# Kernel optimization log

Measured on AMD Instinct MI355X. Metric: run time of the kernel, lower is better.

## Reference

```python
import jax, jax.numpy as jnp
import numpy as np

B, D, N, OUT, H = 32768, 256, 4, 512, 4
DH = D // H


def _layer_norm(x, g, b, eps=1e-5):
    mu = jnp.mean(x, axis=-1, keepdims=True)
    var = jnp.mean(jnp.square(x - mu), axis=-1, keepdims=True)
    return (x - mu) * jax.lax.rsqrt(var + eps) * g + b


def setup_inputs() -> dict:
    key = jax.random.key(0)
    ks = jax.random.split(key, 32)
    s = lambda i, shape, scale=0.02: (jax.random.normal(ks[i], shape, jnp.float32) * scale)
    inp = {
        'w0': jax.random.normal(ks[0], (B, D), jnp.float32),
        'w1': jax.random.normal(ks[1], (B, D), jnp.float32),
        'w2': jax.random.normal(ks[2], (B, D), jnp.float32),
        'w3': jax.random.normal(ks[3], (B, D), jnp.float32),
        'regime': jax.random.uniform(ks[4], (B, 4), jnp.float32),
        'tf_weights': jnp.array([0.5, 1.0, 1.5, 2.0], jnp.float32),
        'in_proj_w': s(5, (3 * D, D)),
        'in_proj_b': s(6, (3 * D,)),
        'out_proj_w': s(7, (D, D)),
        'out_proj_b': s(8, (D,)),
        'ln1_g': jnp.ones((D,), jnp.float32),
        'ln1_b': jnp.zeros((D,), jnp.float32),
        'sg_w': s(9, (D, 4)),
        'sg_b': s(10, (D,)),
        'sb_w': s(11, (D, 4)),
        'sb_b': s(12, (D,)),
        'f1_w': s(13, (2 * OUT, D * N)),
        'f1_b': s(14, (2 * OUT,)),
        'f2_w': s(15, (OUT, 2 * OUT)),
        'f2_b': s(16, (OUT,)),
        'ln2_g': jnp.ones((OUT,), jnp.float32),
        'ln2_b': jnp.zeros((OUT,), jnp.float32),
        'a1_w': s(17, (128, D * N)),
        'a1_b': s(18, (128,)),
        'a2_w': s(19, (1, 128)),
        'a2_b': s(20, (1,)),
    }
    return inp


def _forward(w0, w1, w2, w3, regime, tf_weights, in_proj_w, in_proj_b,
             out_proj_w, out_proj_b, ln1_g, ln1_b, sg_w, sg_b, sb_w, sb_b,
             f1_w, f1_b, f2_w, f2_b, ln2_g, ln2_b, a1_w, a1_b, a2_w, a2_b):
    weights = jax.nn.softmax(tf_weights)  # [N]
    wav = jnp.stack([w0, w1, w2, w3], axis=1)  # [B, N, D]
    weighted = wav * weights[None, :, None]    # [B, N, D]
    query = weighted[:, 0, :]                  # [B, D]

    # MultiheadAttention: q_len=1, kv_len=N, H heads
    wq, wk, wv = in_proj_w[:D], in_proj_w[D:2 * D], in_proj_w[2 * D:]
    bq, bk, bv = in_proj_b[:D], in_proj_b[D:2 * D], in_proj_b[2 * D:]
    q = (query @ wq.T + bq).reshape(B, H, DH)              # [B, H, Dh]
    k = (weighted @ wk.T + bk).reshape(B, N, H, DH)        # [B, N, H, Dh]
    v = (weighted @ wv.T + bv).reshape(B, N, H, DH)
    scores = jnp.einsum('bhd,bnhd->bhn', q, k) / jnp.sqrt(jnp.float32(DH))
    attn = jax.nn.softmax(scores, axis=-1)                 # [B, H, N]
    ctx = jnp.einsum('bhn,bnhd->bhd', attn, v).reshape(B, D)
    attn_out = ctx @ out_proj_w.T + out_proj_b             # [B, D]

    entry = _layer_norm(query + attn_out, ln1_g, ln1_b)    # [B, D]
    gamma = regime @ sg_w.T + sg_b
    beta = regime @ sb_w.T + sb_b
    entry = entry * (1.0 + gamma) + beta                   # FiLM

    cat = jnp.concatenate([entry, weighted[:, 1, :], weighted[:, 2, :], weighted[:, 3, :]], axis=-1)  # [B, D*N]
    h = jax.nn.gelu(cat @ f1_w.T + f1_b, approximate=False)
    fused = _layer_norm(h @ f2_w.T + f2_b, ln2_g, ln2_b)   # [B, OUT]

    a = jax.nn.gelu(cat @ a1_w.T + a1_b, approximate=False)
    alignment = jax.nn.sigmoid(a @ a2_w.T + a2_b)          # [B, 1]
    return fused, alignment


def reference(w0, w1, w2, w3, regime, tf_weights, in_proj_w, in_proj_b,
              out_proj_w, out_proj_b, ln1_g, ln1_b, sg_w, sg_b, sb_w, sb_b,
              f1_w, f1_b, f2_w, f2_b, ln2_g, ln2_b, a1_w, a1_b, a2_w, a2_b):
    return _forward(w0, w1, w2, w3, regime, tf_weights, in_proj_w, in_proj_b,
                    out_proj_w, out_proj_b, ln1_g, ln1_b, sg_w, sg_b, sb_w, sb_b,
                    f1_w, f1_b, f2_w, f2_b, ln2_g, ln2_b, a1_w, a1_b, a2_w, a2_b)
```

## Files before the change

### kernel.cpp

```cpp
#include <hip/hip_runtime.h>
#include <math.h>

#define NB 32768

typedef unsigned short u16;
typedef __attribute__((ext_vector_type(4))) float f32x4;
typedef __attribute__((ext_vector_type(8))) short bf16x8;

__device__ __forceinline__ float bf2f(u16 u){ return __uint_as_float(((unsigned int)u)<<16); }
__device__ __forceinline__ u16 f2bf(float f){
    unsigned int x = __float_as_uint(f);
    x += 0x7fffu + ((x>>16)&1u);
    return (u16)(x>>16);
}
__device__ __forceinline__ float gelu_f(float x){
    float z = fabsf(x) * 0.70710678118654752f;
    float t = __builtin_amdgcn_rcpf(1.0f + 0.3275911f*z);
    float p = t*(0.254829592f + t*(-0.284496736f + t*(1.421413741f + t*(-1.453152027f + t*1.061405429f))));
    float e = __expf(-z*z);
    float erf_abs = 1.0f - p*e;
    float erfv = copysignf(erf_abs, x);
    return 0.5f*x*(1.0f + erfv);
}

__device__ __forceinline__ void gload16(const void* g, void* l){
    __builtin_amdgcn_global_load_lds(
        (const __attribute__((address_space(1))) unsigned int*)g,
        (__attribute__((address_space(3))) unsigned int*)l, 16, 0, 0);
}

__global__ __launch_bounds__(256) void prepconv_kernel(
    const float* __restrict__ w0, const float* __restrict__ w1,
    const float* __restrict__ w2, const float* __restrict__ w3,
    const float* __restrict__ tfw, u16* __restrict__ wcat,
    const float* __restrict__ ipw_s, u16* __restrict__ ipw_d,
    const float* __restrict__ op_s,  u16* __restrict__ op_d,
    const float* __restrict__ f1_s,  u16* __restrict__ f1_d,
    const float* __restrict__ f2_s,  u16* __restrict__ f2_d,
    const float* __restrict__ a1_s,  u16* __restrict__ a1_d)
{
    const int blk = blockIdx.x, tid = threadIdx.x;
    if (blk < 8192){
        float t0=tfw[0], t1=tfw[1], t2=tfw[2], t3=tfw[3];
        float m = fmaxf(fmaxf(t0,t1), fmaxf(t2,t3));
        float e0=expf(t0-m), e1=expf(t1-m), e2=expf(t2-m), e3=expf(t3-m);
        float inv = 1.0f/(e0+e1+e2+e3);
        float s0=e0*inv, s1=e1*inv, s2=e2*inv, s3=e3*inv;

        int idx = blk*256 + tid;
        int b  = idx >> 6;
        int d4 = (idx & 63) << 2;
        size_t src = (size_t)b*256 + d4;
        float4 a0 = *reinterpret_cast<const float4*>(w0 + src);
        float4 a1 = *reinterpret_cast<const float4*>(w1 + src);
        float4 a2 = *reinterpret_cast<const float4*>(w2 + src);
        float4 a3 = *reinterpret_cast<const float4*>(w3 + src);
        size_t dst = (size_t)b*1024 + d4;
        ushort4 o;
        o.x=f2bf(a0.x*s0); o.y=f2bf(a0.y*s0); o.z=f2bf(a0.z*s0); o.w=f2bf(a0.w*s0);
        *reinterpret_cast<ushort4*>(wcat + dst) = o;
        o.x=f2bf(a1.x*s1); o.y=f2bf(a1.y*s1); o.z=f2bf(a1.z*s1); o.w=f2bf(a1.w*s1);
        *reinterpret_cast<ushort4*>(wcat + dst + 256) = o;
        o.x=f2bf(a2.x*s2); o.y=f2bf(a2.y*s2); o.z=f2bf(a2.z*s2); o.w=f2bf(a2.w*s2);
        *reinterpret_cast<ushort4*>(wcat + dst + 512) = o;
        o.x=f2bf(a3.x*s3); o.y=f2bf(a3.y*s3); o.z=f2bf(a3.z*s3); o.w=f2bf(a3.w*s3);
        *reinterpret_cast<ushort4*>(wcat + dst + 768) = o;
    } else {
        int i = (blk - 8192)*256 + tid;
        const float* s; u16* d; int off;
        if      (i < 49152)  { s=ipw_s; d=ipw_d; off=i; }
        else if (i < 65536)  { s=op_s;  d=op_d;  off=i-49152; }
        else if (i < 327680) { s=f1_s;  d=f1_d;  off=i-65536; }
        else if (i < 458752) { s=f2_s;  d=f2_d;  off=i-327680; }
        else                 { s=a1_s;  d=a1_d;  off=i-458752; }
        float4 v = reinterpret_cast<const float4*>(s)[off];
        ushort4 o; o.x=f2bf(v.x); o.y=f2bf(v.y); o.z=f2bf(v.z); o.w=f2bf(v.w);
        reinterpret_cast<ushort4*>(d)[off] = o;
    }
}

template<int ACT>
__global__ __launch_bounds__(256) void mgemm_kernel(
    const u16* __restrict__ A, int lda,
    const u16* __restrict__ W, int ldw,
    const float* __restrict__ bias,
    u16* __restrict__ C, int ldc, int K,
    const float* __restrict__ a2w, const float* __restrict__ a2b, float* __restrict__ aln)
{
    __shared__ __align__(16) u16 sA[4096];
    __shared__ __align__(16) u16 sB[4096];

    const int tid  = threadIdx.x;
    const int lane = tid & 63;
    const int wid  = tid >> 6;
    const int wr   = wid >> 1, wc = wid & 1;
    const int row0 = blockIdx.x << 7, col0 = blockIdx.y << 7;

    const int e0 = tid << 3,          r0s = e0 >> 5, c0s = e0 & 31;
    const int e1 = (256 + tid) << 3,  r1s = e1 >> 5, c1s = e1 & 31;
    const u16* gA0 = A + (size_t)(row0 + r0s)*lda + c0s;
    const u16* gA1 = A + (size_t)(row0 + r1s)*lda + c1s;
    const u16* gB0 = W + (size_t)(col0 + r0s)*ldw + c0s;
    const u16* gB1 = W + (size_t)(col0 + r1s)*ldw + c1s;
    u16* lA0 = sA + (wid << 9);
    u16* lA1 = sA + 2048 + (wid << 9);
    u16* lB0 = sB + (wid << 9);
    u16* lB1 = sB + 2048 + (wid << 9);

    const int la  = lane & 15;
    const int lk  = (lane >> 4) << 3;
    const int hi4 = (lane >> 4) << 2;
    const u16* rA = sA + (((wr << 6) + la) << 5) + lk;
    const u16* rB = sB + (((wc << 6) + la) << 5) + lk;

    f32x4 acc[4][4];
    {
        f32x4 binit[4];
        #pragma unroll
        for (int n=0;n<4;n++){
            float4 b4 = *reinterpret_cast<const float4*>(bias + col0 + (wc<<6) + (n<<4) + hi4);
            binit[n] = (f32x4){b4.x, b4.y, b4.z, b4.w};
        }
        #pragma unroll
        for (int m=0;m<4;m++)
            #pragma unroll
            for (int n=0;n<4;n++) acc[m][n] = binit[n];
    }

    for (int k0 = 0; k0 < K; k0 += 32){
        gload16(gA0 + k0, lA0);
        gload16(gA1 + k0, lA1);
        gload16(gB0 + k0, lB0);
        gload16(gB1 + k0, lB1);
        __syncthreads();
        bf16x8 af[4], bf[4];
        #pragma unroll
        for (int m=0;m<4;m++) af[m] = *reinterpret_cast<const bf16x8*>(rA + (m << 9));
        #pragma unroll
        for (int n=0;n<4;n++) bf[n] = *reinterpret_cast<const bf16x8*>(rB + (n << 9));
        #pragma unroll
        for (int m=0;m<4;m++)
            #pragma unroll
            for (int n=0;n<4;n++)
                acc[m][n] = __builtin_amdgcn_mfma_f32_16x16x32_bf16(bf[n], af[m], acc[m][n], 0, 0, 0);
        __syncthreads();
    }

    if (ACT == 2){
        float w4[4][4];
        #pragma unroll
        for (int n=0;n<4;n++){
            float4 t4 = *reinterpret_cast<const float4*>(a2w + (wc<<6) + (n<<4) + hi4);
            w4[n][0]=t4.x; w4[n][1]=t4.y; w4[n][2]=t4.z; w4[n][3]=t4.w;
        }
        float* red = reinterpret_cast<float*>(sA);
        #pragma unroll
        for (int m=0;m<4;m++){
            float p = 0.f;
            #pragma unroll
            for (int n=0;n<4;n++){
                f32x4 v = acc[m][n];
                p += gelu_f(v[0])*w4[n][0] + gelu_f(v[1])*w4[n][1]
                   + gelu_f(v[2])*w4[n][2] + gelu_f(v[3])*w4[n][3];
            }
            red[(((wr<<6) + (m<<4) + la) << 3) + (wc<<2) + (lane>>4)] = p;
        }
        __syncthreads();
        if (tid < 128){
            float s = 0.f;
            #pragma unroll
            for (int k2=0;k2<8;k2++) s += red[(tid<<3)+k2];
            aln[row0 + tid] = 1.0f/(1.0f + __expf(-(s + a2b[0])));
        }
        return;
    }

    #pragma unroll
    for (int m=0;m<4;m++){
        const int grow = row0 + (wr << 6) + (m << 4) + la;
        u16* crow = C + (size_t)grow*ldc + col0 + (wc << 6) + hi4;
        #pragma unroll
        for (int n=0;n<4;n++){
            f32x4 v = acc[m][n];
            float x0=v[0], x1=v[1], x2=v[2], x3=v[3];
            if (ACT == 1){ x0=gelu_f(x0); x1=gelu_f(x1); x2=gelu_f(x2); x3=gelu_f(x3); }
            ushort4 o; o.x=f2bf(x0); o.y=f2bf(x1); o.z=f2bf(x2); o.w=f2bf(x3);
            *reinterpret_cast<ushort4*>(crow + (n << 4)) = o;
        }
    }
}

template<int ACT>
__global__ __launch_bounds__(512) void gemm256p_kernel(
    const u16* __restrict__ A, int lda,
    const u16* __restrict__ W, int ldw,
    const float* __restrict__ bias,
    u16* __restrict__ C, int ldc, int K)
{
    __shared__ __align__(16) u16 sT[65536];

    const int tid  = threadIdx.x;
    const int lane = tid & 63;
    const int wid  = tid >> 6;
    const int wr   = wid >> 2;
    const int wc   = wid & 3;
    const int row0 = blockIdx.x << 8, col0 = blockIdx.y << 8;

    const int la = lane & 15;
    const int hi = lane >> 4;

    f32x4 acc[8][4];
    {
        f32x4 binit[4];
        #pragma unroll
        for (int n=0;n<4;n++){
            float4 b4 = *reinterpret_cast<const float4*>(bias + col0 + (wc<<6) + (n<<4) + (hi<<2));
            binit[n] = (f32x4){b4.x, b4.y, b4.z, b4.w};
        }
        #pragma unroll
        for (int m=0;m<8;m++)
            #pragma unroll
            for (int n=0;n<4;n++) acc[m][n] = binit[n];
    }

    const int rs = (wid << 4) + (lane >> 3);
    const int cs = ((lane & 7) ^ ((lane >> 3) & 7)) << 3;
    const u16* gA0 = A + (size_t)(row0 + rs)*lda + cs;
    const u16* gA1 = gA0 + (size_t)128*lda;
    const u16* gB0 = W + (size_t)(col0 + rs)*ldw + cs;
    const u16* gB1 = gB0 + (size_t)128*ldw;
    const int ldsw = (wid << 4) * 64;

    const int cph0 = (hi ^ (la & 7)) << 3;
    const u16* rAbase = sT + ((wr << 7) + la)*64;
    const u16* rBbase = sT + 16384 + ((wc << 6) + la)*64;

    const int NT = K >> 6;

    gload16(gB0, sT + 16384 + ldsw);          gload16(gB0 + 8*(size_t)ldw, sT + 16384 + ldsw + 512);
    gload16(gB1, sT + 24576 + ldsw);          gload16(gB1 + 8*(size_t)ldw, sT + 24576 + ldsw + 512);
    gload16(gA0, sT + ldsw);                  gload16(gA0 + 8*(size_t)lda, sT + ldsw + 512);
    gload16(gA1, sT + 8192 + ldsw);           gload16(gA1 + 8*(size_t)lda, sT + 8192 + ldsw + 512);

#define STG(GP, LD, DOFF) \
        gload16(GP + kb, sT + bn + (DOFF) + ldsw); \
        gload16(GP + kb + 8*(size_t)(LD), sT + bn + (DOFF) + ldsw + 512);

#define DSRA(MH, CO) { \
        const u16* rA_ = rAbase + b + ((MH) << 12) + (CO); \
        af[0] = *reinterpret_cast<const bf16x8*>(rA_); \
        af[1] = *reinterpret_cast<const bf16x8*>(rA_ + 1024); \
        af[2] = *reinterpret_cast<const bf16x8*>(rA_ + 2048); \
        af[3] = *reinterpret_cast<const bf16x8*>(rA_ + 3072); }

#define DSRB(CO) { \
        const u16* rB_ = rBbase + b + (CO); \
        bf[0] = *reinterpret_cast<const bf16x8*>(rB_); \
        bf[1] = *reinterpret_cast<const bf16x8*>(rB_ + 1024); \
        bf[2] = *reinterpret_cast<const bf16x8*>(rB_ + 2048); \
        bf[3] = *reinterpret_cast<const bf16x8*>(rB_ + 3072); }

#define MFMA16(MB) { \
        _Pragma("unroll") \
        for (int m=0;m<4;m++){ \
            _Pragma("unroll") \
            for (int n=0;n<4;n++) \
                acc[(MB)+m][n] = __builtin_amdgcn_mfma_f32_16x16x32_bf16(bf[n], af[m], acc[(MB)+m][n], 0,0,0); \
        } }

    for (int t = 0; t < NT; ++t){
        const int b  = (t & 1) << 15;
        const int bn = b ^ 32768;
        const bool stg = (t + 1 < NT);
        const int kb = (t + 1) << 6;
        bf16x8 af[4], bf[4];
        const int co0 = cph0;
        const int co1 = cph0 ^ 32;

        asm volatile("s_waitcnt vmcnt(0)" ::: "memory");
        __builtin_amdgcn_s_barrier();
        __builtin_amdgcn_sched_barrier(0);
        DSRB(co0)
        DSRA(0, co0)
        if (stg){ STG(gB0, ldw, 16384) }
        MFMA16(0)
        DSRA(1, co0)
        if (stg){ STG(gB1, ldw, 24576) }
        __builtin_amdgcn_sched_barrier(0);
        __builtin_amdgcn_s_barrier();
        __builtin_amdgcn_sched_barrier(0);
        MFMA16(4)
        DSRB(co1)
        DSRA(0, co1)
        if (stg){ STG(gA0, lda, 0) }
        __builtin_amdgcn_sched_barrier(0);
        __builtin_amdgcn_s_barrier();
        __builtin_amdgcn_sched_barrier(0);
        MFMA16(0)
        DSRA(1, co1)
        if (stg){ STG(gA1, lda, 8192) }
        __builtin_amdgcn_sched_barrier(0);
        __builtin_amdgcn_s_barrier();
        __builtin_amdgcn_sched_barrier(0);
        MFMA16(4)
    }
#undef STG
#undef DSRA
#undef DSRB
#undef MFMA16

    #pragma unroll
    for (int m=0;m<8;m++){
        const int grow = row0 + (wr << 7) + (m << 4) + la;
        u16* crow = C + (size_t)grow*ldc + col0 + (wc << 6) + (hi << 2);
        #pragma unroll
        for (int n=0;n<4;n++){
            f32x4 v = acc[m][n];
            float x0=v[0], x1=v[1], x2=v[2], x3=v[3];
            if (ACT == 1){ x0=gelu_f(x0); x1=gelu_f(x1); x2=gelu_f(x2); x3=gelu_f(x3); }
            ushort4 o; o.x=f2bf(x0); o.y=f2bf(x1); o.z=f2bf(x2); o.w=f2bf(x3);
            *reinterpret_cast<ushort4*>(crow + (n << 4)) = o;
        }
    }
}

__global__ __launch_bounds__(256) void attn_kernel(
    const u16* __restrict__ q, const u16* __restrict__ kv,
    u16* __restrict__ ctx)
{
    __shared__ float sQ[256], sK[1024], sV[1024], sS[16], sA[16];
    const int b = blockIdx.x, t = threadIdx.x;
    sQ[t] = bf2f(q[(size_t)b*256 + t]);
    #pragma unroll
    for (int n=0;n<4;n++){
        sK[n*256+t] = bf2f(kv[(size_t)b*2048 + n*512 + t]);
        sV[n*256+t] = bf2f(kv[(size_t)b*2048 + n*512 + 256 + t]);
    }
    __syncthreads();
    if (t < 16){
        int h = t>>2, n = t&3;
        float s = 0.f;
        const int o = h*64;
        #pragma unroll
        for (int dh=0; dh<64; ++dh) s += sQ[o+dh]*sK[n*256+o+dh];
        sS[t] = s * 0.125f;
    }
    __syncthreads();
    if (t < 4){
        float a0=sS[t*4+0], a1=sS[t*4+1], a2=sS[t*4+2], a3=sS[t*4+3];
        float m = fmaxf(fmaxf(a0,a1), fmaxf(a2,a3));
        float e0=expf(a0-m), e1=expf(a1-m), e2=expf(a2-m), e3=expf(a3-m);
        float inv = 1.0f/(e0+e1+e2+e3);
        sA[t*4+0]=e0*inv; sA[t*4+1]=e1*inv; sA[t*4+2]=e2*inv; sA[t*4+3]=e3*inv;
    }
    __syncthreads();
    const int h = t>>6;
    float c = sA[h*4+0]*sV[t] + sA[h*4+1]*sV[256+t] + sA[h*4+2]*sV[512+t] + sA[h*4+3]*sV[768+t];
    ctx[(size_t)b*256 + t] = f2bf(c);
}

__global__ __launch_bounds__(256) void lnfilm_kernel(
    u16* __restrict__ wcat, const u16* __restrict__ ao, const float* __restrict__ regime,
    const float* __restrict__ sgw, const float* __restrict__ sgb,
    const float* __restrict__ sbw, const float* __restrict__ sbb,
    const float* __restrict__ g1, const float* __restrict__ b1)
{
    const int b = blockIdx.x, t = threadIdx.x;
    float x = bf2f(wcat[(size_t)b*1024 + t]) + bf2f(ao[(size_t)b*256 + t]);
    float s = x, q = x*x;
    #pragma unroll
    for (int o=32;o;o>>=1){ s += __shfl_xor(s,o); q += __shfl_xor(q,o); }
    __shared__ float rs[4], rq[4];
    if ((t&63)==0){ rs[t>>6]=s; rq[t>>6]=q; }
    __syncthreads();
    s = rs[0]+rs[1]+rs[2]+rs[3];
    q = rq[0]+rq[1]+rq[2]+rq[3];
    float mu  = s*(1.0f/256.0f);
    float var = q*(1.0f/256.0f) - mu*mu;
    float rstd = rsqrtf(var + 1e-5f);
    float r0=regime[b*4+0], r1=regime[b*4+1], r2=regime[b*4+2], r3=regime[b*4+3];
    float gam = r0*sgw[t*4+0]+r1*sgw[t*4+1]+r2*sgw[t*4+2]+r3*sgw[t*4+3]+sgb[t];
    float bet = r0*sbw[t*4+0]+r1*sbw[t*4+1]+r2*sbw[t*4+2]+r3*sbw[t*4+3]+sbb[t];
    float e = ((x-mu)*rstd*g1[t]+b1[t])*(1.0f+gam)+bet;
    wcat[(size_t)b*1024 + t] = f2bf(e);
}

__global__ __launch_bounds__(256) void ln2_kernel(
    const u16* __restrict__ t1, const float* __restrict__ g, const float* __restrict__ bt,
    float* __restrict__ out)
{
    const int b = blockIdx.x, t = threadIdx.x;
    float x0 = bf2f(t1[(size_t)b*512 + t]);
    float x1 = bf2f(t1[(size_t)b*512 + 256 + t]);
    float s = x0+x1, q = x0*x0 + x1*x1;
    #pragma unroll
    for (int o=32;o;o>>=1){ s += __shfl_xor(s,o); q += __shfl_xor(q,o); }
    __shared__ float rs[4], rq[4];
    if ((t&63)==0){ rs[t>>6]=s; rq[t>>6]=q; }
    __syncthreads();
    s = rs[0]+rs[1]+rs[2]+rs[3];
    q = rq[0]+rq[1]+rq[2]+rq[3];
    float mu  = s*(1.0f/512.0f);
    float var = q*(1.0f/512.0f) - mu*mu;
    float rstd = rsqrtf(var + 1e-5f);
    out[(size_t)b*512 + t]       = (x0-mu)*rstd*g[t]     + bt[t];
    out[(size_t)b*512 + 256 + t] = (x1-mu)*rstd*g[256+t] + bt[256+t];
}

extern "C" void kernel_launch(void* const* d_in, const int* in_sizes, int n_in,
                              void* d_out, int out_size, void* d_ws, size_t ws_size,
                              hipStream_t stream) {
    const float* w0   = (const float*)d_in[0];
    const float* w1   = (const float*)d_in[1];
    const float* w2   = (const float*)d_in[2];
    const float* w3   = (const float*)d_in[3];
    const float* regime = (const float*)d_in[4];
    const float* tfw  = (const float*)d_in[5];
    const float* in_proj_w = (const float*)d_in[6];
    const float* in_proj_b = (const float*)d_in[7];
    const float* out_proj_w = (const float*)d_in[8];
    const float* out_proj_b = (const float*)d_in[9];
    const float* ln1_g = (const float*)d_in[10];
    const float* ln1_b = (const float*)d_in[11];
    const float* sg_w = (const float*)d_in[12];
    const float* sg_b = (const float*)d_in[13];
    const float* sb_w = (const float*)d_in[14];
    const float* sb_b = (const float*)d_in[15];
    const float* f1_w = (const float*)d_in[16];
    const float* f1_b = (const float*)d_in[17];
    const float* f2_w = (const float*)d_in[18];
    const float* f2_b = (const float*)d_in[19];
    const float* ln2_g = (const float*)d_in[20];
    const float* ln2_b = (const float*)d_in[21];
    const float* a1_w = (const float*)d_in[22];
    const float* a1_b = (const float*)d_in[23];
    const float* a2_w = (const float*)d_in[24];
    const float* a2_b = (const float*)d_in[25];

    char* ws = (char*)d_ws;
    u16* wcat  = (u16*)(ws);
    u16* qbuf  = (u16*)(ws + 67108864ull);
    u16* kvbuf = (u16*)(ws + 83886080ull);
    u16* hbuf  = kvbuf;
    u16* t1buf = (u16*)(ws + 150994944ull);
    u16* aobuf = (u16*)(ws + 184549376ull);
    u16* wb    = (u16*)(ws + 218103808ull);
    u16* ipw = wb;
    u16* opw = wb + 196608;
    u16* f1w = wb + 262144;
    u16* f2w = wb + 1310720;
    u16* a1w = wb + 1835008;

    float* out_fused = (float*)d_out;
    float* out_align = (float*)d_out + (size_t)NB*512;

    prepconv_kernel<<<10112, 256, 0, stream>>>(w0,w1,w2,w3,tfw,wcat,
        in_proj_w,ipw, out_proj_w,opw, f1_w,f1w, f2_w,f2w, a1_w,a1w);
    mgemm_kernel<0><<<dim3(256, 2), 256, 0, stream>>>(wcat, 1024, ipw, 256, in_proj_b, qbuf, 256, 256, nullptr, nullptr, nullptr);
    gemm256p_kernel<0><<<dim3(512, 2), 512, 0, stream>>>(wcat, 256, ipw+65536, 256, in_proj_b+256, kvbuf, 512, 256);
    attn_kernel<<<NB, 256, 0, stream>>>(qbuf, kvbuf, qbuf);
    mgemm_kernel<0><<<dim3(256, 2), 256, 0, stream>>>(qbuf, 256, opw, 256, out_proj_b, aobuf, 256, 256, nullptr, nullptr, nullptr);
    lnfilm_kernel<<<NB, 256, 0, stream>>>(wcat, aobuf, regime, sg_w, sg_b, sb_w, sb_b, ln1_g, ln1_b);
    gemm256p_kernel<1><<<dim3(128, 4), 512, 0, stream>>>(wcat, 1024, f1w, 1024, f1_b, hbuf, 1024, 1024);
    gemm256p_kernel<0><<<dim3(128, 2), 512, 0, stream>>>(hbuf, 1024, f2w, 1024, f2_b, t1buf, 512, 1024);
    ln2_kernel<<<NB, 256, 0, stream>>>(t1buf, ln2_g, ln2_b, out_fused);
    mgemm_kernel<2><<<dim3(256, 1), 256, 0, stream>>>(wcat, 1024, a1w, 1024, a1_b, qbuf, 128, 1024, a2_w, a2_b, out_align);
}
```

Baseline: 353.8 us.

## Fuse attention, out-projection GEMM and LayerNorm+FiLM into one kernel

Replaces three launches (per-row attention, out_proj GEMM, LN1+FiLM) with one kernel that handles 16 rows per block. It stages K/V and Q in LDS, computes scores and softmax with shuffles, and builds the context in LDS. It then runs the out-projection with MFMA against the bf16 weights read from global memory, and applies residual, LayerNorm and FiLM in place. This removes the global round trips for ctx and attn_out plus two launches, at the cost of about 73KB of LDS per block, which limits occupancy, and each block rereading the full out_proj weight.

Result: faster. 342.6 us (-3.1%).

```diff
diff --git a/kernel.cpp b/kernel.cpp
--- a/kernel.cpp
+++ b/kernel.cpp
@@ -324,65 +324,119 @@
     }
 }
 
-__global__ __launch_bounds__(256) void attn_kernel(
+__global__ __launch_bounds__(256) void attnop_kernel(
     const u16* __restrict__ q, const u16* __restrict__ kv,
-    u16* __restrict__ ctx)
-{
-    __shared__ float sQ[256], sK[1024], sV[1024], sS[16], sA[16];
-    const int b = blockIdx.x, t = threadIdx.x;
-    sQ[t] = bf2f(q[(size_t)b*256 + t]);
-    #pragma unroll
-    for (int n=0;n<4;n++){
-        sK[n*256+t] = bf2f(kv[(size_t)b*2048 + n*512 + t]);
-        sV[n*256+t] = bf2f(kv[(size_t)b*2048 + n*512 + 256 + t]);
-    }
-    __syncthreads();
-    if (t < 16){
-        int h = t>>2, n = t&3;
-        float s = 0.f;
-        const int o = h*64;
-        #pragma unroll
-        for (int dh=0; dh<64; ++dh) s += sQ[o+dh]*sK[n*256+o+dh];
-        sS[t] = s * 0.125f;
-    }
-    __syncthreads();
-    if (t < 4){
-        float a0=sS[t*4+0], a1=sS[t*4+1], a2=sS[t*4+2], a3=sS[t*4+3];
-        float m = fmaxf(fmaxf(a0,a1), fmaxf(a2,a3));
-        float e0=expf(a0-m), e1=expf(a1-m), e2=expf(a2-m), e3=expf(a3-m);
-        float inv = 1.0f/(e0+e1+e2+e3);
-        sA[t*4+0]=e0*inv; sA[t*4+1]=e1*inv; sA[t*4+2]=e2*inv; sA[t*4+3]=e3*inv;
-    }
-    __syncthreads();
-    const int h = t>>6;
-    float c = sA[h*4+0]*sV[t] + sA[h*4+1]*sV[256+t] + sA[h*4+2]*sV[512+t] + sA[h*4+3]*sV[768+t];
-    ctx[(size_t)b*256 + t] = f2bf(c);
-}
-
-__global__ __launch_bounds__(256) void lnfilm_kernel(
-    u16* __restrict__ wcat, const u16* __restrict__ ao, const float* __restrict__ regime,
+    u16* __restrict__ wcat,
+    const u16* __restrict__ opw, const float* __restrict__ opb,
+    const float* __restrict__ regime,
     const float* __restrict__ sgw, const float* __restrict__ sgb,
     const float* __restrict__ sbw, const float* __restrict__ sbb,
     const float* __restrict__ g1, const float* __restrict__ b1)
 {
-    const int b = blockIdx.x, t = threadIdx.x;
-    float x = bf2f(wcat[(size_t)b*1024 + t]) + bf2f(ao[(size_t)b*256 + t]);
-    float s = x, q = x*x;
-    #pragma unroll
-    for (int o=32;o;o>>=1){ s += __shfl_xor(s,o); q += __shfl_xor(q,o); }
-    __shared__ float rs[4], rq[4];
-    if ((t&63)==0){ rs[t>>6]=s; rq[t>>6]=q; }
+    __shared__ __align__(16) u16 sKV[32768];
+    __shared__ __align__(16) u16 sQC[16*264];
+    __shared__ float sAT[256];
+
+    const int t  = threadIdx.x;
+    const int b0 = blockIdx.x << 4;
+
+    {
+        const int row = t >> 4, u = t & 15;
+        const u16* qsrc = q + (size_t)(b0 + row)*256 + (u << 4);
+        *reinterpret_cast<bf16x8*>(sQC + row*264 + (u<<4))     = *reinterpret_cast<const bf16x8*>(qsrc);
+        *reinterpret_cast<bf16x8*>(sQC + row*264 + (u<<4) + 8) = *reinterpret_cast<const bf16x8*>(qsrc + 8);
+        const u16* kvsrc = kv + (size_t)b0*2048;
+        #pragma unroll
+        for (int j=0;j<16;j++){
+            const int off = (t<<3) + j*2048;
+            *reinterpret_cast<bf16x8*>(sKV + off) = *reinterpret_cast<const bf16x8*>(kvsrc + off);
+        }
+    }
     __syncthreads();
-    s = rs[0]+rs[1]+rs[2]+rs[3];
-    q = rq[0]+rq[1]+rq[2]+rq[3];
-    float mu  = s*(1.0f/256.0f);
-    float var = q*(1.0f/256.0f) - mu*mu;
-    float rstd = rsqrtf(var + 1e-5f);
-    float r0=regime[b*4+0], r1=regime[b*4+1], r2=regime[b*4+2], r3=regime[b*4+3];
-    float gam = r0*sgw[t*4+0]+r1*sgw[t*4+1]+r2*sgw[t*4+2]+r3*sgw[t*4+3]+sgb[t];
-    float bet = r0*sbw[t*4+0]+r1*sbw[t*4+1]+r2*sbw[t*4+2]+r3*sbw[t*4+3]+sbb[t];
-    float e = ((x-mu)*rstd*g1[t]+b1[t])*(1.0f+gam)+bet;
-    wcat[(size_t)b*1024 + t] = f2bf(e);
+
+    {
+        const int s = t >> 4, h = (t >> 2) & 3, n = t & 3;
+        float sc = 0.f;
+        const u16* qp = sQC + s*264 + h*64;
+        const u16* kp = sKV + s*2048 + n*512 + h*64;
+        #pragma unroll
+        for (int dh=0; dh<64; ++dh) sc += bf2f(qp[dh]) * bf2f(kp[dh]);
+        sc *= 0.125f;
+        float m = fmaxf(sc, __shfl_xor(sc, 1)); m = fmaxf(m, __shfl_xor(m, 2));
+        float e = __expf(sc - m);
+        float sum = e + __shfl_xor(e, 1); sum += __shfl_xor(sum, 2);
+        sAT[t] = e / sum;
+    }
+    __syncthreads();
+
+    {
+        const int s = t >> 4, u = t & 15;
+        #pragma unroll
+        for (int j=0;j<16;j++){
+            const int d = (u << 4) + j;
+            const int h = d >> 6;
+            const float* a = sAT + s*16 + (h<<2);
+            const u16* vp = sKV + s*2048 + 256 + d;
+            float c = a[0]*bf2f(vp[0]) + a[1]*bf2f(vp[512]) + a[2]*bf2f(vp[1024]) + a[3]*bf2f(vp[1536]);
+            sQC[s*264 + d] = f2bf(c);
+        }
+    }
+    __syncthreads();
+
+    float* sAO = reinterpret_cast<float*>(sKV);
+    {
+        const int lane = t & 63, wid = t >> 6;
+        const int la = lane & 15, hi = lane >> 4;
+        f32x4 acc[4];
+        #pragma unroll
+        for (int n=0;n<4;n++){
+            float4 b4 = *reinterpret_cast<const float4*>(opb + (wid<<6) + (n<<4) + (hi<<2));
+            acc[n] = (f32x4){b4.x, b4.y, b4.z, b4.w};
+        }
+        #pragma unroll
+        for (int ks=0; ks<8; ++ks){
+            bf16x8 af = *reinterpret_cast<const bf16x8*>(sQC + la*264 + (ks<<5) + (hi<<3));
+            #pragma unroll
+            for (int n=0;n<4;n++){
+                bf16x8 wf = *reinterpret_cast<const bf16x8*>(
+                    opw + (size_t)((wid<<6) + (n<<4) + la)*256 + (ks<<5) + (hi<<3));
+                acc[n] = __builtin_amdgcn_mfma_f32_16x16x32_bf16(wf, af, acc[n], 0, 0, 0);
+            }
+        }
+        #pragma unroll
+        for (int n=0;n<4;n++){
+            float4 st = {acc[n][0], acc[n][1], acc[n][2], acc[n][3]};
+            *reinterpret_cast<float4*>(sAO + la*264 + (wid<<6) + (n<<4) + (hi<<2)) = st;
+        }
+    }
+    __syncthreads();
+
+    {
+        const int s = t >> 4, u = t & 15;
+        u16* qrow = wcat + (size_t)(b0 + s)*1024;
+        float xv[16], sum = 0.f, sq = 0.f;
+        #pragma unroll
+        for (int j=0;j<16;j++){
+            const int d = u + (j << 4);
+            float x = sAO[s*264 + d] + bf2f(qrow[d]);
+            xv[j] = x; sum += x; sq += x*x;
+        }
+        #pragma unroll
+        for (int o=1;o<16;o<<=1){ sum += __shfl_xor(sum, o); sq += __shfl_xor(sq, o); }
+        float mu   = sum * (1.0f/256.0f);
+        float var  = sq  * (1.0f/256.0f) - mu*mu;
+        float rstd = rsqrtf(var + 1e-5f);
+        const float r0 = regime[(b0+s)*4+0], r1 = regime[(b0+s)*4+1];
+        const float r2 = regime[(b0+s)*4+2], r3 = regime[(b0+s)*4+3];
+        #pragma unroll
+        for (int j=0;j<16;j++){
+            const int d = u + (j << 4);
+            float gam = r0*sgw[d*4+0] + r1*sgw[d*4+1] + r2*sgw[d*4+2] + r3*sgw[d*4+3] + sgb[d];
+            float bet = r0*sbw[d*4+0] + r1*sbw[d*4+1] + r2*sbw[d*4+2] + r3*sbw[d*4+3] + sbb[d];
+            float e = ((xv[j]-mu)*rstd*g1[d] + b1[d])*(1.0f+gam) + bet;
+            qrow[d] = f2bf(e);
+        }
+    }
 }
 
 __global__ __launch_bounds__(256) void ln2_kernel(
@@ -443,7 +497,6 @@
     u16* kvbuf = (u16*)(ws + 83886080ull);
     u16* hbuf  = kvbuf;
     u16* t1buf = (u16*)(ws + 150994944ull);
-    u16* aobuf = (u16*)(ws + 184549376ull);
     u16* wb    = (u16*)(ws + 218103808ull);
     u16* ipw = wb;
     u16* opw = wb + 196608;
@@ -458,9 +511,8 @@
         in_proj_w,ipw, out_proj_w,opw, f1_w,f1w, f2_w,f2w, a1_w,a1w);
     mgemm_kernel<0><<<dim3(256, 2), 256, 0, stream>>>(wcat, 1024, ipw, 256, in_proj_b, qbuf, 256, 256, nullptr, nullptr, nullptr);
     gemm256p_kernel<0><<<dim3(512, 2), 512, 0, stream>>>(wcat, 256, ipw+65536, 256, in_proj_b+256, kvbuf, 512, 256);
-    attn_kernel<<<NB, 256, 0, stream>>>(qbuf, kvbuf, qbuf);
-    mgemm_kernel<0><<<dim3(256, 2), 256, 0, stream>>>(qbuf, 256, opw, 256, out_proj_b, aobuf, 256, 256, nullptr, nullptr, nullptr);
-    lnfilm_kernel<<<NB, 256, 0, stream>>>(wcat, aobuf, regime, sg_w, sg_b, sb_w, sb_b, ln1_g, ln1_b);
+    attnop_kernel<<<2048, 256, 0, stream>>>(qbuf, kvbuf, wcat, opw, out_proj_b,
+        regime, sg_w, sg_b, sb_w, sb_b, ln1_g, ln1_b);
     gemm256p_kernel<1><<<dim3(128, 4), 512, 0, stream>>>(wcat, 1024, f1w, 1024, f1_b, hbuf, 1024, 1024);
     gemm256p_kernel<0><<<dim3(128, 2), 512, 0, stream>>>(hbuf, 1024, f2w, 1024, f2_b, t1buf, 512, 1024);
     ln2_kernel<<<NB, 256, 0, stream>>>(t1buf, ln2_g, ln2_b, out_fused);
```
